# Performance work log

Measured on AMD Instinct MI355X. Metric: run time of the kernel, lower is better.

## Reference

```python
import jax, jax.numpy as jnp
import numpy as np

LN_EPS = 1e-5

def _layernorm(x, gamma, beta):
    mu = jnp.mean(x, axis=-1, keepdims=True)
    var = jnp.var(x, axis=-1, keepdims=True)
    return (x - mu) * jax.lax.rsqrt(var + LN_EPS) * gamma + beta

def setup_inputs() -> dict:
    key = jax.random.key(0)
    ks = jax.random.split(key, 4)
    B, s, d, L = 8, 192, 512, 8
    h = 2048  # embed_dim * 2
    return {
        "lags": jax.random.normal(ks[0], (B, s, d, L), dtype=jnp.float32),
        "gamma1": jnp.ones((d,), jnp.float32),
        "beta1": jnp.zeros((d,), jnp.float32),
        "W1": jax.random.normal(ks[1], (d, h), jnp.float32) * (1.0 / np.sqrt(d)),
        "b1": jnp.zeros((h,), jnp.float32),
        "W2": jax.random.normal(ks[2], (h, d), jnp.float32) * (1.0 / np.sqrt(h)),
        "b2": jnp.zeros((d,), jnp.float32),
        "gamma3": jnp.ones((d,), jnp.float32),
        "beta3": jnp.zeros((d,), jnp.float32),
    }

def reference(lags, gamma1, beta1, W1, b1, W2, b2, gamma3, beta3):
    B, s, d, L = lags.shape
    # (B, s, d, L) -> (B, s, L, d) -> (B, S=s*L, d)
    x = jnp.transpose(lags, (0, 1, 3, 2)).reshape(B, s * L, d)
    scale = 1.0 / jnp.sqrt(jnp.asarray(d, x.dtype))
    # single-head, unprojected attention: scores = X X^T / sqrt(d)
    scores = jnp.einsum('bqd,bkd->bqk', x, x) * scale  # [B, S, S]
    attn = jax.nn.softmax(scores, axis=-1)
    attn_out = jnp.einsum('bqk,bkd->bqd', attn, x)
    q = _layernorm(x + attn_out, gamma1, beta1)
    ff = jnp.dot(jax.nn.gelu(jnp.dot(q, W1) + b1, approximate=False), W2) + b2
    out = _layernorm(q + ff, gamma3, beta3)
    # (B, S, d) -> (B, s, L, d) -> (B, s, d, L)
    return jnp.transpose(out.reshape(B, s, L, d), (0, 1, 3, 2))
```

## Files before the change

### kernel.cpp

```cpp
#include <hip/hip_runtime.h>
#include <hip/hip_bf16.h>
#include <math.h>

#define B_ 8
#define S_ 192
#define D_ 512
#define L_ 8
#define SQ 1536
#define H_ 2048
#define NROW (B_*SQ)
#define SCALE_QK 0.04419417382415922f

typedef unsigned short ushort_t;
typedef unsigned int uint_t;
typedef __attribute__((ext_vector_type(8))) short bf16x8;
typedef __attribute__((ext_vector_type(4))) float f32x4;
typedef __attribute__((ext_vector_type(16))) float f32x16;

__device__ __forceinline__ float bfu2f(ushort_t u) { return __uint_as_float((unsigned)u << 16); }
__device__ __forceinline__ ushort_t f2bfu(float f) {
  __hip_bfloat16 h = __float2bfloat16(f);
  return *reinterpret_cast<ushort_t*>(&h);
}

__device__ __forceinline__ float gelu_tanh(float x) {
  float x2 = x * x;
  float u2 = x * fmaf(0.0713548162f, x2, 1.5957691216f);
  float e = __expf(u2);
  float r = fmaf(-2.0f, __builtin_amdgcn_rcpf(e + 1.0f), 1.0f);
  float hx = 0.5f * x;
  return fmaf(hx, r, hx);
}

__device__ __forceinline__ void gl_lds16(const ushort_t* g, ushort_t* l) {
  __builtin_amdgcn_global_load_lds(
      (const __attribute__((address_space(1))) unsigned int*)g,
      (__attribute__((address_space(3))) unsigned int*)l, 16, 0, 0);
}

#define VMWAIT(N) asm volatile("s_waitcnt vmcnt(" #N ")" ::: "memory")

__global__ __launch_bounds__(256) void k_build_x_f(const float* __restrict__ lags,
                                                   float* __restrict__ x,
                                                   ushort_t* __restrict__ x_bf,
                                                   ushort_t* __restrict__ xT) {
  __shared__ float tile[512][9];
  const int tid = threadIdx.x;
  const float* in = lags + (size_t)blockIdx.x * 4096;
  #pragma unroll
  for (int it = 0; it < 4; ++it) {
    int f = (tid + it * 256) * 4;
    float4 v = *reinterpret_cast<const float4*>(in + f);
    int k = f >> 3, l0 = f & 7;
    tile[k][l0] = v.x; tile[k][l0 + 1] = v.y; tile[k][l0 + 2] = v.z; tile[k][l0 + 3] = v.w;
  }
  __syncthreads();
  const int l = tid >> 5, kbase = tid & 31;
  const size_t r = (size_t)blockIdx.x * 8 + l;
  #pragma unroll
  for (int j = 0; j < 16; ++j) {
    int k = kbase + 32 * j;
    float v = tile[k][l];
    x[r * D_ + k] = v;
    x_bf[r * D_ + k] = f2bfu(v);
  }
  const int b = blockIdx.x / S_, si = blockIdx.x - b * S_;
  #pragma unroll
  for (int dd = 0; dd < 2; ++dd) {
    int d = tid + dd * 256;
    uint_t pk[4];
    #pragma unroll
    for (int j = 0; j < 4; ++j) {
      uint_t lo = f2bfu(tile[d][2 * j]);
      uint_t hi = f2bfu(tile[d][2 * j + 1]);
      pk[j] = (hi << 16) | lo;
    }
    uint_t* dst = (uint_t*)(xT + ((size_t)b * D_ + d) * SQ + si * 8);
    *reinterpret_cast<uint4*>(dst) = make_uint4(pk[0], pk[1], pk[2], pk[3]);
  }
}

__global__ __launch_bounds__(256) void k_wt(const float* __restrict__ W,
                                            ushort_t* __restrict__ Wt,
                                            int K, int N) {
  __shared__ ushort_t tile[64][65];
  int n0 = blockIdx.x * 64, k0 = blockIdx.y * 64;
  for (int i = threadIdx.x; i < 4096; i += 256) {
    int kk = i >> 6, nn = i & 63;
    tile[nn][kk] = f2bfu(W[(size_t)(k0 + kk) * N + n0 + nn]);
  }
  __syncthreads();
  for (int i = threadIdx.x; i < 4096; i += 256) {
    int nn = i >> 6, kk = i & 63;
    Wt[(size_t)(n0 + nn) * K + k0 + kk] = tile[nn][kk];
  }
}

template<int MODE>
__global__ __launch_bounds__(256) void k_gemm(const ushort_t* __restrict__ A,
                                              const ushort_t* __restrict__ Bt,
                                              const float* __restrict__ bias,
                                              void* __restrict__ Cout,
                                              int M, int K, int N,
                                              size_t sAz, size_t sBz, size_t sCz,
                                              float scale) {
  A  += (size_t)blockIdx.z * sAz;
  Bt += (size_t)blockIdx.z * sBz;
  __shared__ ushort_t As0[128 * 64];
  __shared__ ushort_t As1[128 * 64];
  __shared__ ushort_t Bs0[128 * 64];
  __shared__ ushort_t Bs1[128 * 64];
  const int tid = threadIdx.x;
  const int m0 = blockIdx.y * 128, n0 = blockIdx.x * 128;
  const int w = tid >> 6, lane = tid & 63;
  const int wr = w >> 1, wc = w & 1;
  const int l31 = lane & 31, khi = lane >> 5, x7 = lane & 7;
  const int lrow8 = lane >> 3;
  const int cg = ((lane & 7) ^ lrow8) * 8;
  const int lbase = (w * 32) * 64;
  const size_t sK8 = (size_t)8 * K;

  f32x16 acc[2][2];
  if (MODE <= 1) {
    #pragma unroll
    for (int nj = 0; nj < 2; ++nj) {
      float bv = bias[n0 + wc * 64 + nj * 32 + l31];
      #pragma unroll
      for (int mi = 0; mi < 2; ++mi)
        #pragma unroll
        for (int rg = 0; rg < 16; ++rg) acc[mi][nj][rg] = bv;
    }
  } else {
    #pragma unroll
    for (int nj = 0; nj < 2; ++nj)
      #pragma unroll
      for (int mi = 0; mi < 2; ++mi)
        #pragma unroll
        for (int rg = 0; rg < 16; ++rg) acc[mi][nj][rg] = 0.f;
  }

  const ushort_t* gA = A  + (size_t)(m0 + w * 32 + lrow8) * K + cg;
  const ushort_t* gB = Bt + (size_t)(n0 + w * 32 + lrow8) * K + cg;

#define STAGE(AS, BS) do {                                                  \
    ushort_t* la_ = &AS[lbase]; ushort_t* lb_ = &BS[lbase];                 \
    _Pragma("unroll")                                                       \
    for (int j_ = 0; j_ < 4; ++j_) {                                        \
      gl_lds16(gA + (size_t)j_ * sK8, la_ + j_ * 8 * 64);                   \
      gl_lds16(gB + (size_t)j_ * sK8, lb_ + j_ * 8 * 64);                   \
    }                                                                       \
    gA += 64; gB += 64;                                                     \
  } while (0)

#define COMPUTE(AS, BS) do {                                                \
    _Pragma("unroll")                                                       \
    for (int ks_ = 0; ks_ < 4; ++ks_) {                                     \
      const int pos_ = ((ks_ * 2 + khi) ^ x7) * 8;                          \
      bf16x8 af_[2], bf_[2];                                                \
      _Pragma("unroll")                                                     \
      for (int mi_ = 0; mi_ < 2; ++mi_)                                     \
        af_[mi_] = *reinterpret_cast<const bf16x8*>(                        \
            &AS[(wr * 64 + mi_ * 32 + l31) * 64 + pos_]);                   \
      _Pragma("unroll")                                                     \
      for (int nj_ = 0; nj_ < 2; ++nj_)                                     \
        bf_[nj_] = *reinterpret_cast<const bf16x8*>(                        \
            &BS[(wc * 64 + nj_ * 32 + l31) * 64 + pos_]);                   \
      _Pragma("unroll")                                                     \
      for (int mi_ = 0; mi_ < 2; ++mi_)                                     \
        _Pragma("unroll")                                                   \
        for (int nj_ = 0; nj_ < 2; ++nj_)                                   \
          acc[mi_][nj_] = __builtin_amdgcn_mfma_f32_32x32x16_bf16(          \
              af_[mi_], bf_[nj_], acc[mi_][nj_], 0, 0, 0);                  \
    }                                                                       \
  } while (0)

  STAGE(As0, Bs0);
  STAGE(As1, Bs1);

  const int nt = K >> 6;
  for (int t = 0; t < nt - 2; t += 2) {
    VMWAIT(8);
    __builtin_amdgcn_s_barrier();
    COMPUTE(As0, Bs0);
    __builtin_amdgcn_s_barrier();
    STAGE(As0, Bs0);
    VMWAIT(8);
    __builtin_amdgcn_s_barrier();
    COMPUTE(As1, Bs1);
    __builtin_amdgcn_s_barrier();
    STAGE(As1, Bs1);
  }
  VMWAIT(8);
  __builtin_amdgcn_s_barrier();
  COMPUTE(As0, Bs0);
  VMWAIT(0);
  __builtin_amdgcn_s_barrier();
  COMPUTE(As1, Bs1);

#undef STAGE
#undef COMPUTE

  ushort_t* Cb = (ushort_t*)Cout + (size_t)blockIdx.z * sCz;
  float*    Cf = (float*)Cout    + (size_t)blockIdx.z * sCz;
  #pragma unroll
  for (int mi = 0; mi < 2; ++mi)
    #pragma unroll
    for (int nj = 0; nj < 2; ++nj) {
      int gc = n0 + wc * 64 + nj * 32 + l31;
      #pragma unroll
      for (int rg = 0; rg < 16; ++rg) {
        int gr = m0 + wr * 64 + mi * 32 + (rg & 3) + 8 * (rg >> 2) + 4 * khi;
        float v = acc[mi][nj][rg];
        if (MODE == 0) {
          Cb[(size_t)gr * N + gc] = f2bfu(gelu_tanh(v));
        } else if (MODE == 1) {
          Cf[(size_t)gr * N + gc] = v;
        } else if (MODE == 2) {
          Cb[(size_t)gr * N + gc] = f2bfu(v * scale);
        } else {
          Cf[(size_t)gr * N + gc] = v;
        }
      }
    }
}

__global__ __launch_bounds__(256) void k_softmax_bf(ushort_t* __restrict__ sc) {
  uint_t* row = (uint_t*)(sc + (size_t)blockIdx.z * SQ * SQ + (size_t)blockIdx.x * SQ);
  int tid = threadIdx.x;
  __shared__ float red[8];
  float v[6];
  float m = -1e30f;
  #pragma unroll
  for (int k = 0; k < 3; ++k) {
    uint_t u = row[tid + k * 256];
    v[2*k]   = __uint_as_float(u << 16);
    v[2*k+1] = __uint_as_float(u & 0xffff0000u);
    m = fmaxf(m, fmaxf(v[2*k], v[2*k+1]));
  }
  #pragma unroll
  for (int o = 32; o > 0; o >>= 1) m = fmaxf(m, __shfl_down(m, o));
  if ((tid & 63) == 0) red[tid >> 6] = m;
  __syncthreads();
  m = fmaxf(fmaxf(red[0], red[1]), fmaxf(red[2], red[3]));
  __syncthreads();
  float ssum = 0.f;
  #pragma unroll
  for (int k = 0; k < 6; ++k) { v[k] = expf(v[k] - m); ssum += v[k]; }
  #pragma unroll
  for (int o = 32; o > 0; o >>= 1) ssum += __shfl_down(ssum, o);
  if ((tid & 63) == 0) red[4 + (tid >> 6)] = ssum;
  __syncthreads();
  float inv = 1.0f / (red[4] + red[5] + red[6] + red[7]);
  #pragma unroll
  for (int k = 0; k < 3; ++k) {
    uint_t lo = f2bfu(v[2*k] * inv);
    uint_t hi = f2bfu(v[2*k+1] * inv);
    row[tid + k * 256] = (hi << 16) | lo;
  }
}

__global__ __launch_bounds__(256) void k_ln1b(const float* __restrict__ x,
                                              const float* __restrict__ attn,
                                              const float* __restrict__ g,
                                              const float* __restrict__ be,
                                              ushort_t* __restrict__ qbf) {
  size_t base = (size_t)blockIdx.x * D_;
  int tid = threadIdx.x;
  __shared__ float rl[8];
  float v0 = x[base + tid] + attn[base + tid];
  float v1 = x[base + tid + 256] + attn[base + tid + 256];
  float s = v0 + v1, sq = v0 * v0 + v1 * v1;
  #pragma unroll
  for (int o = 32; o > 0; o >>= 1) { s += __shfl_down(s, o); sq += __shfl_down(sq, o); }
  int lane = tid & 63, wid = tid >> 6;
  if (lane == 0) { rl[wid] = s; rl[4 + wid] = sq; }
  __syncthreads();
  s = rl[0] + rl[1] + rl[2] + rl[3];
  sq = rl[4] + rl[5] + rl[6] + rl[7];
  float mean = s * (1.0f / 512.0f);
  float var = sq * (1.0f / 512.0f) - mean * mean;
  float rstd = rsqrtf(var + 1e-5f);
  qbf[base + tid]       = f2bfu((v0 - mean) * rstd * g[tid] + be[tid]);
  qbf[base + tid + 256] = f2bfu((v1 - mean) * rstd * g[tid + 256] + be[tid + 256]);
}

__global__ __launch_bounds__(256) void k_ln3_f(const float* __restrict__ y,
                                               const ushort_t* __restrict__ qbf,
                                               const float* __restrict__ g3,
                                               const float* __restrict__ be3,
                                               float* __restrict__ out) {
  __shared__ float ynorm[8][512];
  const int tid = threadIdx.x;
  const int w = tid >> 6, lane = tid & 63;
  #pragma unroll
  for (int rr = 0; rr < 2; ++rr) {
    int l = 2 * w + rr;
    size_t t = (size_t)blockIdx.x * 8 + l;
    float v[8];
    float s = 0.f, sq = 0.f;
    #pragma unroll
    for (int j = 0; j < 8; ++j) {
      int k = lane + 64 * j;
      v[j] = y[t * D_ + k] + bfu2f(qbf[t * D_ + k]);
      s += v[j]; sq += v[j] * v[j];
    }
    #pragma unroll
    for (int o = 32; o > 0; o >>= 1) { s += __shfl_down(s, o); sq += __shfl_down(sq, o); }
    s = __shfl(s, 0); sq = __shfl(sq, 0);
    float mean = s * (1.0f / 512.0f);
    float var = sq * (1.0f / 512.0f) - mean * mean;
    float rstd = rsqrtf(var + 1e-5f);
    #pragma unroll
    for (int j = 0; j < 8; ++j) {
      int k = lane + 64 * j;
      ynorm[l][k] = (v[j] - mean) * rstd * g3[k] + be3[k];
    }
  }
  __syncthreads();
  float* ob = out + (size_t)blockIdx.x * 4096;
  #pragma unroll
  for (int kk = 0; kk < 2; ++kk) {
    int k = tid * 2 + kk;
    float4 lo = make_float4(ynorm[0][k], ynorm[1][k], ynorm[2][k], ynorm[3][k]);
    float4 hi = make_float4(ynorm[4][k], ynorm[5][k], ynorm[6][k], ynorm[7][k]);
    *reinterpret_cast<float4*>(ob + (size_t)k * 8)     = lo;
    *reinterpret_cast<float4*>(ob + (size_t)k * 8 + 4) = hi;
  }
}

#define TS 64
#define KT 16
__global__ __launch_bounds__(256) void k_build_x_s(const float* __restrict__ lags,
                                                   float* __restrict__ x, int b_base) {
  int idx = blockIdx.x * 256 + threadIdx.x;
  int k = idx & (D_ - 1);
  int r = idx >> 9;
  int b = b_base + r / SQ;
  int t = r - (r / SQ) * SQ;
  int si = t >> 3, l = t & 7;
  size_t src = (((size_t)(b * S_ + si) * D_ + k) << 3) + l;
  x[idx] = lags[src];
}

__global__ __launch_bounds__(256) void k_scores(const float* __restrict__ x,
                                                float* __restrict__ sc, int b_base) {
  const float* A = x;
  float* C = sc;
  __shared__ float As[TS][KT + 1];
  __shared__ float Bs[TS][KT + 1];
  int tx = threadIdx.x & 15, ty = threadIdx.x >> 4;
  int j0 = blockIdx.x * TS, i0 = blockIdx.y * TS;
  float acc[4][4] = {};
  int lk = threadIdx.x & 15, lr = threadIdx.x >> 4;
  for (int k0 = 0; k0 < D_; k0 += KT) {
    #pragma unroll
    for (int it = 0; it < 4; ++it) {
      As[lr + 16 * it][lk] = A[(size_t)(i0 + lr + 16 * it) * D_ + k0 + lk];
      Bs[lr + 16 * it][lk] = A[(size_t)(j0 + lr + 16 * it) * D_ + k0 + lk];
    }
    __syncthreads();
    #pragma unroll
    for (int kk = 0; kk < KT; ++kk) {
      float a[4], bb[4];
      #pragma unroll
      for (int r = 0; r < 4; ++r) a[r] = As[ty * 4 + r][kk];
      #pragma unroll
      for (int c = 0; c < 4; ++c) bb[c] = Bs[tx * 4 + c][kk];
      #pragma unroll
      for (int r = 0; r < 4; ++r)
        #pragma unroll
        for (int c = 0; c < 4; ++c) acc[r][c] = fmaf(a[r], bb[c], acc[r][c]);
    }
    __syncthreads();
  }
  #pragma unroll
  for (int r = 0; r < 4; ++r) {
    float4 v = make_float4(acc[r][0]*SCALE_QK, acc[r][1]*SCALE_QK,
                           acc[r][2]*SCALE_QK, acc[r][3]*SCALE_QK);
    *reinterpret_cast<float4*>(&C[(size_t)(i0 + ty*4 + r) * SQ + j0 + tx*4]) = v;
  }
}

__global__ __launch_bounds__(256) void k_softmax(float* __restrict__ sc) {
  float* row = sc + (size_t)blockIdx.x * SQ;
  int tid = threadIdx.x;
  __shared__ float red[8];
  float m = -1e30f;
  for (int j = tid; j < SQ; j += 256) m = fmaxf(m, row[j]);
  #pragma unroll
  for (int o = 32; o > 0; o >>= 1) m = fmaxf(m, __shfl_down(m, o));
  if ((tid & 63) == 0) red[tid >> 6] = m;
  __syncthreads();
  m = fmaxf(fmaxf(red[0], red[1]), fmaxf(red[2], red[3]));
  __syncthreads();
  float ssum = 0.f;
  for (int j = tid; j < SQ; j += 256) { float e = expf(row[j] - m); row[j] = e; ssum += e; }
  #pragma unroll
  for (int o = 32; o > 0; o >>= 1) ssum += __shfl_down(ssum, o);
  if ((tid & 63) == 0) red[4 + (tid >> 6)] = ssum;
  __syncthreads();
  float inv = 1.0f / (red[4] + red[5] + red[6] + red[7]);
  for (int j = tid; j < SQ; j += 256) row[j] *= inv;
}

__global__ __launch_bounds__(256) void k_attn(const float* __restrict__ x,
                                              const float* __restrict__ sc,
                                              float* __restrict__ attn) {
  const float* X = x;
  const float* P = sc;
  float* O = attn;
  __shared__ float Ps[TS][KT + 1];
  __shared__ float Xs[KT][TS];
  int tx = threadIdx.x & 15, ty = threadIdx.x >> 4;
  int j0 = blockIdx.x * TS, i0 = blockIdx.y * TS;
  float acc[4][4] = {};
  int lk = threadIdx.x & 15, lr = threadIdx.x >> 4;
  int lc = threadIdx.x & 63, lrow = threadIdx.x >> 6;
  for (int k0 = 0; k0 < SQ; k0 += KT) {
    #pragma unroll
    for (int it = 0; it < 4; ++it)
      Ps[lr + 16 * it][lk] = P[(size_t)(i0 + lr + 16 * it) * SQ + k0 + lk];
    #pragma unroll
    for (int it = 0; it < 4; ++it)
      Xs[lrow + 4 * it][lc] = X[(size_t)(k0 + lrow + 4 * it) * D_ + j0 + lc];
    __syncthreads();
    #pragma unroll
    for (int kk = 0; kk < KT; ++kk) {
      float a[4], bb[4];
      #pragma unroll
      for (int r = 0; r < 4; ++r) a[r] = Ps[ty * 4 + r][kk];
      #pragma unroll
      for (int c = 0; c < 4; ++c) bb[c] = Xs[kk][tx * 4 + c];
      #pragma unroll
      for (int r = 0; r < 4; ++r)
        #pragma unroll
        for (int c = 0; c < 4; ++c) acc[r][c] = fmaf(a[r], bb[c], acc[r][c]);
    }
    __syncthreads();
  }
  #pragma unroll
  for (int r = 0; r < 4; ++r) {
    float4 v = make_float4(acc[r][0], acc[r][1], acc[r][2], acc[r][3]);
    *reinterpret_cast<float4*>(&O[(size_t)(i0 + ty*4 + r) * D_ + j0 + tx*4]) = v;
  }
}

__global__ __launch_bounds__(256) void k_ln1(const float* __restrict__ x,
                                             const float* __restrict__ attn,
                                             const float* __restrict__ g,
                                             const float* __restrict__ be,
                                             float* __restrict__ qout) {
  size_t base = (size_t)blockIdx.x * D_;
  int tid = threadIdx.x;
  __shared__ float rl[8];
  float v0 = x[base + tid] + attn[base + tid];
  float v1 = x[base + tid + 256] + attn[base + tid + 256];
  float s = v0 + v1, sq = v0 * v0 + v1 * v1;
  #pragma unroll
  for (int o = 32; o > 0; o >>= 1) { s += __shfl_down(s, o); sq += __shfl_down(sq, o); }
  int lane = tid & 63, wid = tid >> 6;
  if (lane == 0) { rl[wid] = s; rl[4 + wid] = sq; }
  __syncthreads();
  s = rl[0] + rl[1] + rl[2] + rl[3];
  sq = rl[4] + rl[5] + rl[6] + rl[7];
  float mean = s * (1.0f / 512.0f);
  float var = sq * (1.0f / 512.0f) - mean * mean;
  float rstd = rsqrtf(var + 1e-5f);
  qout[base + tid]       = (v0 - mean) * rstd * g[tid] + be[tid];
  qout[base + tid + 256] = (v1 - mean) * rstd * g[tid + 256] + be[tid + 256];
}

__global__ __launch_bounds__(256, 2) void k_ffn(
    const float* __restrict__ q,
    const float* __restrict__ W1, const float* __restrict__ b1,
    const float* __restrict__ W2, const float* __restrict__ b2,
    const float* __restrict__ g3, const float* __restrict__ be3,
    float* __restrict__ out, int row_base)
{
  __shared__ float qs[8][D_];
  __shared__ float mid[8][H_];
  const int tid = threadIdx.x;
  const int row0 = blockIdx.x * 8;
  for (int idx = tid; idx < 8 * D_; idx += 256)
    qs[idx >> 9][idx & (D_ - 1)] = q[(size_t)row0 * D_ + idx];
  __syncthreads();
  float acc[8][8];
  {
    float4 bA = *reinterpret_cast<const float4*>(b1 + (tid << 3));
    float4 bB = *reinterpret_cast<const float4*>(b1 + (tid << 3) + 4);
    float bv[8] = {bA.x, bA.y, bA.z, bA.w, bB.x, bB.y, bB.z, bB.w};
    #pragma unroll
    for (int jj = 0; jj < 8; ++jj)
      #pragma unroll
      for (int r = 0; r < 8; ++r) acc[jj][r] = bv[jj];
  }
  for (int k4 = 0; k4 < D_ / 4; ++k4) {
    float4 qv[8];
    #pragma unroll
    for (int r = 0; r < 8; ++r)
      qv[r] = *reinterpret_cast<const float4*>(&qs[r][k4 << 2]);
    #pragma unroll
    for (int kk = 0; kk < 4; ++kk) {
      const int k = (k4 << 2) + kk;
      float4 wA = *reinterpret_cast<const float4*>(W1 + (size_t)k * H_ + (tid << 3));
      float4 wB = *reinterpret_cast<const float4*>(W1 + (size_t)k * H_ + (tid << 3) + 4);
      float wv[8] = {wA.x, wA.y, wA.z, wA.w, wB.x, wB.y, wB.z, wB.w};
      #pragma unroll
      for (int r = 0; r < 8; ++r) {
        float qk = (kk == 0) ? qv[r].x : (kk == 1) ? qv[r].y : (kk == 2) ? qv[r].z : qv[r].w;
        #pragma unroll
        for (int jj = 0; jj < 8; ++jj) acc[jj][r] = fmaf(qk, wv[jj], acc[jj][r]);
      }
    }
  }
  #pragma unroll
  for (int jj = 0; jj < 8; ++jj)
    #pragma unroll
    for (int r = 0; r < 8; ++r) {
      float v = acc[jj][r];
      mid[r][(tid << 3) + jj] = 0.5f * v * (1.0f + erff(v * 0.70710678118654752f));
    }
  __syncthreads();
  float acc2[8][2];
  {
    float b20 = b2[tid << 1], b21 = b2[(tid << 1) + 1];
    #pragma unroll
    for (int r = 0; r < 8; ++r) { acc2[r][0] = b20; acc2[r][1] = b21; }
  }
  for (int j4 = 0; j4 < H_ / 4; ++j4) {
    float4 mv[8];
    #pragma unroll
    for (int r = 0; r < 8; ++r)
      mv[r] = *reinterpret_cast<const float4*>(&mid[r][j4 << 2]);
    #pragma unroll
    for (int kk = 0; kk < 4; ++kk) {
      const int j = (j4 << 2) + kk;
      float2 wv = *reinterpret_cast<const float2*>(W2 + (size_t)j * D_ + (tid << 1));
      #pragma unroll
      for (int r = 0; r < 8; ++r) {
        float m = (kk == 0) ? mv[r].x : (kk == 1) ? mv[r].y : (kk == 2) ? mv[r].z : mv[r].w;
        acc2[r][0] = fmaf(m, wv.x, acc2[r][0]);
        acc2[r][1] = fmaf(m, wv.y, acc2[r][1]);
      }
    }
  }
  __syncthreads();
  float* ys = &mid[0][0];
  #pragma unroll
  for (int r = 0; r < 8; ++r) {
    ys[r * D_ + (tid << 1)]     = qs[r][(tid << 1)]     + acc2[r][0];
    ys[r * D_ + (tid << 1) + 1] = qs[r][(tid << 1) + 1] + acc2[r][1];
  }
  __syncthreads();
  float g3a = g3[tid],  g3b = g3[tid + 256];
  float be3a = be3[tid], be3b = be3[tid + 256];
  float* rl = &qs[0][0];
  for (int r = 0; r < 8; ++r) {
    float v0 = ys[r * D_ + tid], v1 = ys[r * D_ + tid + 256];
    float s = v0 + v1, sq = v0 * v0 + v1 * v1;
    #pragma unroll
    for (int o = 32; o > 0; o >>= 1) { s += __shfl_down(s, o); sq += __shfl_down(sq, o); }
    int lane = tid & 63, wid = tid >> 6;
    if (lane == 0) { rl[wid] = s; rl[4 + wid] = sq; }
    __syncthreads();
    s = rl[0] + rl[1] + rl[2] + rl[3];
    sq = rl[4] + rl[5] + rl[6] + rl[7];
    __syncthreads();
    float mean = s * (1.0f / 512.0f);
    float var = sq * (1.0f / 512.0f) - mean * mean;
    float rstd = rsqrtf(var + 1e-5f);
    int t = row_base + row0 + r;
    int b = t / SQ, tt = t - b * SQ;
    int si = tt >> 3, l = tt & 7;
    size_t ob = (((size_t)(b * S_ + si) * D_) << 3) + l;
    out[ob + ((size_t)tid << 3)]         = (v0 - mean) * rstd * g3a + be3a;
    out[ob + ((size_t)(tid + 256) << 3)] = (v1 - mean) * rstd * g3b + be3b;
  }
}

extern "C" void kernel_launch(void* const* d_in, const int* in_sizes, int n_in,
                              void* d_out, int out_size, void* d_ws, size_t ws_size,
                              hipStream_t stream) {
  const float* lags   = (const float*)d_in[0];
  const float* gamma1 = (const float*)d_in[1];
  const float* beta1  = (const float*)d_in[2];
  const float* W1     = (const float*)d_in[3];
  const float* b1     = (const float*)d_in[4];
  const float* W2     = (const float*)d_in[5];
  const float* b2     = (const float*)d_in[6];
  const float* g3     = (const float*)d_in[7];
  const float* be3    = (const float*)d_in[8];
  float* out = (float*)d_out;

  float* ws = (float*)d_ws;
  const size_t NX  = (size_t)B_ * SQ * D_;
  const size_t NXB = (size_t)SQ * D_;
  const size_t NS  = (size_t)SQ * SQ;

  const size_t need_full = (3 * NX + 8 * NS) * sizeof(float);

  if (ws_size >= need_full) {
    float* x        = ws;
    float* attn     = x + NX;
    ushort_t* q_bf  = (ushort_t*)(attn + NX);
    ushort_t* w1t   = q_bf + NX;
    ushort_t* w2t   = w1t + (size_t)H_ * D_;
    ushort_t* region = w2t + (size_t)H_ * D_;
    ushort_t* sc_bf = region;
    ushort_t* x_bf  = region + 8 * NS;
    ushort_t* xT_bf = x_bf + NX;
    ushort_t* mid_bf = region;

    k_build_x_f<<<dim3(B_ * S_), 256, 0, stream>>>(lags, x, x_bf, xT_bf);
    k_wt<<<dim3(H_ / 64, D_ / 64), 256, 0, stream>>>(W1, w1t, D_, H_);
    k_wt<<<dim3(D_ / 64, H_ / 64), 256, 0, stream>>>(W2, w2t, H_, D_);
    k_gemm<2><<<dim3(SQ / 128, SQ / 128, B_), 256, 0, stream>>>(
        x_bf, x_bf, nullptr, sc_bf, SQ, D_, SQ, NXB, NXB, NS, SCALE_QK);
    k_softmax_bf<<<dim3(SQ, 1, B_), 256, 0, stream>>>(sc_bf);
    k_gemm<3><<<dim3(D_ / 128, SQ / 128, B_), 256, 0, stream>>>(
        sc_bf, xT_bf, nullptr, attn, SQ, SQ, D_, NS, NXB, NXB, 1.0f);
    k_ln1b<<<dim3(NROW), 256, 0, stream>>>(x, attn, gamma1, beta1, q_bf);
    k_gemm<0><<<dim3(H_ / 128, NROW / 128, 1), 256, 0, stream>>>(
        q_bf, w1t, b1, mid_bf, NROW, D_, H_, 0, 0, 0, 1.0f);
    k_gemm<1><<<dim3(D_ / 128, NROW / 128, 1), 256, 0, stream>>>(
        mid_bf, w2t, b2, attn, NROW, H_, D_, 0, 0, 0, 1.0f);
    k_ln3_f<<<dim3(B_ * S_), 256, 0, stream>>>(attn, q_bf, g3, be3, out);
  } else {
    float* xb   = ws;
    float* sc   = xb + NXB;
    float* atb  = sc + NS;
    float* qb   = atb + NXB;
    for (int b = 0; b < B_; ++b) {
      k_build_x_s<<<dim3((unsigned)(NXB / 256)), 256, 0, stream>>>(lags, xb, b);
      k_scores<<<dim3(SQ / TS, SQ / TS, 1), 256, 0, stream>>>(xb, sc, b);
      k_softmax<<<dim3(SQ, 1, 1), 256, 0, stream>>>(sc);
      k_attn<<<dim3(D_ / TS, SQ / TS, 1), 256, 0, stream>>>(xb, sc, atb);
      k_ln1<<<dim3(SQ), 256, 0, stream>>>(xb, atb, gamma1, beta1, qb);
      k_ffn<<<dim3(SQ / 8), 256, 0, stream>>>(qb, W1, b1, W2, b2, g3, be3, out, b * SQ);
    }
  }
}
```

Measured before the change: 298.0 us.

## Use 256x128 tiles, 3-stage pipeline, 16x16 MFMA and XCD-aware block remap in GEMMs

Replaces the 128x128 two-buffer GEMM with a 512-thread kernel computing 256x128 tiles. It uses a triple-buffered LDS pipeline with a single barrier per k-step, 16x16x32 bf16 MFMA instead of 32x32x16, and a block-index swizzle that groups tiles by XCD. The aim is to raise operand reuse per block and overlap global loads with compute better. The cost is more LDS per block (144 KB), which lowers occupancy, and fewer blocks for the small attention GEMMs, which may underfill the CUs.

```diff
diff --git a/kernel.cpp b/kernel.cpp
--- a/kernel.cpp
+++ b/kernel.cpp
@@ -15,7 +15,6 @@
 typedef unsigned int uint_t;
 typedef __attribute__((ext_vector_type(8))) short bf16x8;
 typedef __attribute__((ext_vector_type(4))) float f32x4;
-typedef __attribute__((ext_vector_type(16))) float f32x16;
 
 __device__ __forceinline__ float bfu2f(ushort_t u) { return __uint_as_float((unsigned)u << 16); }
 __device__ __forceinline__ ushort_t f2bfu(float f) {
@@ -97,120 +96,122 @@
 }
 
 template<int MODE>
-__global__ __launch_bounds__(256) void k_gemm(const ushort_t* __restrict__ A,
-                                              const ushort_t* __restrict__ Bt,
-                                              const float* __restrict__ bias,
-                                              void* __restrict__ Cout,
-                                              int M, int K, int N,
-                                              size_t sAz, size_t sBz, size_t sCz,
-                                              float scale) {
+__global__ __launch_bounds__(512) void k_gemm2(const ushort_t* __restrict__ A,
+                                               const ushort_t* __restrict__ Bt,
+                                               const float* __restrict__ bias,
+                                               void* __restrict__ Cout,
+                                               int M, int K, int N,
+                                               size_t sAz, size_t sBz, size_t sCz,
+                                               float scale) {
   A  += (size_t)blockIdx.z * sAz;
   Bt += (size_t)blockIdx.z * sBz;
-  __shared__ ushort_t As0[128 * 64];
-  __shared__ ushort_t As1[128 * 64];
+  __shared__ ushort_t As0[256 * 64];
+  __shared__ ushort_t As1[256 * 64];
+  __shared__ ushort_t As2[256 * 64];
   __shared__ ushort_t Bs0[128 * 64];
   __shared__ ushort_t Bs1[128 * 64];
+  __shared__ ushort_t Bs2[128 * 64];
+
+  const int gx = gridDim.x;
+  const int nwg = gx * gridDim.y;
+  int lin = blockIdx.y * gx + blockIdx.x;
+  lin = (lin & 7) * (nwg >> 3) + (lin >> 3);
+  const int n0 = (lin % gx) * 128;
+  const int m0 = (lin / gx) * 256;
+
   const int tid = threadIdx.x;
-  const int m0 = blockIdx.y * 128, n0 = blockIdx.x * 128;
   const int w = tid >> 6, lane = tid & 63;
-  const int wr = w >> 1, wc = w & 1;
-  const int l31 = lane & 31, khi = lane >> 5, x7 = lane & 7;
+  const int wm = w >> 1, wn = w & 1;
+  const int l15 = lane & 15, quad = lane >> 4;
   const int lrow8 = lane >> 3;
   const int cg = ((lane & 7) ^ lrow8) * 8;
-  const int lbase = (w * 32) * 64;
-  const size_t sK8 = (size_t)8 * K;
-
-  f32x16 acc[2][2];
+  const int xsw = l15 & 7;
+  const size_t sK64 = (size_t)64 * K;
+
+  f32x4 acc[4][4];
   if (MODE <= 1) {
     #pragma unroll
-    for (int nj = 0; nj < 2; ++nj) {
-      float bv = bias[n0 + wc * 64 + nj * 32 + l31];
-      #pragma unroll
-      for (int mi = 0; mi < 2; ++mi)
-        #pragma unroll
-        for (int rg = 0; rg < 16; ++rg) acc[mi][nj][rg] = bv;
+    for (int nj = 0; nj < 4; ++nj) {
+      float bv = bias[n0 + wn * 64 + nj * 16 + l15];
+      #pragma unroll
+      for (int mi = 0; mi < 4; ++mi) acc[mi][nj] = (f32x4){bv, bv, bv, bv};
     }
   } else {
     #pragma unroll
-    for (int nj = 0; nj < 2; ++nj)
-      #pragma unroll
-      for (int mi = 0; mi < 2; ++mi)
-        #pragma unroll
-        for (int rg = 0; rg < 16; ++rg) acc[mi][nj][rg] = 0.f;
-  }
-
-  const ushort_t* gA = A  + (size_t)(m0 + w * 32 + lrow8) * K + cg;
-  const ushort_t* gB = Bt + (size_t)(n0 + w * 32 + lrow8) * K + cg;
-
-#define STAGE(AS, BS) do {                                                  \
-    ushort_t* la_ = &AS[lbase]; ushort_t* lb_ = &BS[lbase];                 \
-    _Pragma("unroll")                                                       \
-    for (int j_ = 0; j_ < 4; ++j_) {                                        \
-      gl_lds16(gA + (size_t)j_ * sK8, la_ + j_ * 8 * 64);                   \
-      gl_lds16(gB + (size_t)j_ * sK8, lb_ + j_ * 8 * 64);                   \
-    }                                                                       \
-    gA += 64; gB += 64;                                                     \
+    for (int nj = 0; nj < 4; ++nj)
+      #pragma unroll
+      for (int mi = 0; mi < 4; ++mi) acc[mi][nj] = (f32x4){0.f, 0.f, 0.f, 0.f};
+  }
+
+  const ushort_t* pA = A  + (size_t)(m0 + w * 8 + lrow8) * K + cg;
+  const ushort_t* pB = Bt + (size_t)(n0 + w * 8 + lrow8) * K + cg;
+  const int lb = (w * 8) * 64;
+
+#define STAGE(TT, AS, BS) do {                                              \
+    const size_t ko_ = (size_t)(TT) * 64;                                   \
+    gl_lds16(pA + ko_,             &AS[lb]);                                \
+    gl_lds16(pA + ko_ +     sK64,  &AS[lb + 64 * 64]);                      \
+    gl_lds16(pA + ko_ + 2 * sK64,  &AS[lb + 128 * 64]);                     \
+    gl_lds16(pA + ko_ + 3 * sK64,  &AS[lb + 192 * 64]);                     \
+    gl_lds16(pB + ko_,             &BS[lb]);                                \
+    gl_lds16(pB + ko_ +     sK64,  &BS[lb + 64 * 64]);                      \
   } while (0)
 
 #define COMPUTE(AS, BS) do {                                                \
     _Pragma("unroll")                                                       \
-    for (int ks_ = 0; ks_ < 4; ++ks_) {                                     \
-      const int pos_ = ((ks_ * 2 + khi) ^ x7) * 8;                          \
-      bf16x8 af_[2], bf_[2];                                                \
+    for (int kk_ = 0; kk_ < 2; ++kk_) {                                     \
+      const int csel_ = ((kk_ * 4 + quad) ^ xsw) * 8;                       \
+      bf16x8 af_[4], bf_[4];                                                \
       _Pragma("unroll")                                                     \
-      for (int mi_ = 0; mi_ < 2; ++mi_)                                     \
+      for (int mi_ = 0; mi_ < 4; ++mi_)                                     \
         af_[mi_] = *reinterpret_cast<const bf16x8*>(                        \
-            &AS[(wr * 64 + mi_ * 32 + l31) * 64 + pos_]);                   \
+            &AS[(wm * 64 + mi_ * 16 + l15) * 64 + csel_]);                  \
       _Pragma("unroll")                                                     \
-      for (int nj_ = 0; nj_ < 2; ++nj_)                                     \
+      for (int nj_ = 0; nj_ < 4; ++nj_)                                     \
         bf_[nj_] = *reinterpret_cast<const bf16x8*>(                        \
-            &BS[(wc * 64 + nj_ * 32 + l31) * 64 + pos_]);                   \
+            &BS[(wn * 64 + nj_ * 16 + l15) * 64 + csel_]);                  \
       _Pragma("unroll")                                                     \
-      for (int mi_ = 0; mi_ < 2; ++mi_)                                     \
+      for (int mi_ = 0; mi_ < 4; ++mi_)                                     \
         _Pragma("unroll")                                                   \
-        for (int nj_ = 0; nj_ < 2; ++nj_)                                   \
-          acc[mi_][nj_] = __builtin_amdgcn_mfma_f32_32x32x16_bf16(          \
+        for (int nj_ = 0; nj_ < 4; ++nj_)                                   \
+          acc[mi_][nj_] = __builtin_amdgcn_mfma_f32_16x16x32_bf16(          \
               af_[mi_], bf_[nj_], acc[mi_][nj_], 0, 0, 0);                  \
     }                                                                       \
   } while (0)
 
-  STAGE(As0, Bs0);
-  STAGE(As1, Bs1);
+#define STEP(TT, CA, CB, NA, NB) do {                                       \
+    if ((TT) < nt) {                                                        \
+      if ((TT) == nt - 1) { VMWAIT(0); } else { VMWAIT(6); }                \
+      __builtin_amdgcn_s_barrier();                                         \
+      if ((TT) + 2 < nt) STAGE((TT) + 2, NA, NB);                           \
+      COMPUTE(CA, CB);                                                      \
+    }                                                                       \
+  } while (0)
 
   const int nt = K >> 6;
-  for (int t = 0; t < nt - 2; t += 2) {
-    VMWAIT(8);
-    __builtin_amdgcn_s_barrier();
-    COMPUTE(As0, Bs0);
-    __builtin_amdgcn_s_barrier();
-    STAGE(As0, Bs0);
-    VMWAIT(8);
-    __builtin_amdgcn_s_barrier();
-    COMPUTE(As1, Bs1);
-    __builtin_amdgcn_s_barrier();
-    STAGE(As1, Bs1);
-  }
-  VMWAIT(8);
-  __builtin_amdgcn_s_barrier();
-  COMPUTE(As0, Bs0);
-  VMWAIT(0);
-  __builtin_amdgcn_s_barrier();
-  COMPUTE(As1, Bs1);
+  STAGE(0, As0, Bs0);
+  STAGE(1, As1, Bs1);
+  for (int t = 0; t < nt; t += 3) {
+    STEP(t,     As0, Bs0, As2, Bs2);
+    STEP(t + 1, As1, Bs1, As0, Bs0);
+    STEP(t + 2, As2, Bs2, As1, Bs1);
+  }
 
 #undef STAGE
 #undef COMPUTE
+#undef STEP
 
   ushort_t* Cb = (ushort_t*)Cout + (size_t)blockIdx.z * sCz;
   float*    Cf = (float*)Cout    + (size_t)blockIdx.z * sCz;
   #pragma unroll
-  for (int mi = 0; mi < 2; ++mi)
-    #pragma unroll
-    for (int nj = 0; nj < 2; ++nj) {
-      int gc = n0 + wc * 64 + nj * 32 + l31;
-      #pragma unroll
-      for (int rg = 0; rg < 16; ++rg) {
-        int gr = m0 + wr * 64 + mi * 32 + (rg & 3) + 8 * (rg >> 2) + 4 * khi;
-        float v = acc[mi][nj][rg];
+  for (int mi = 0; mi < 4; ++mi)
+    #pragma unroll
+    for (int nj = 0; nj < 4; ++nj) {
+      int gc = n0 + wn * 64 + nj * 16 + l15;
+      #pragma unroll
+      for (int r = 0; r < 4; ++r) {
+        int gr = m0 + wm * 64 + mi * 16 + quad * 4 + r;
+        float v = acc[mi][nj][r];
         if (MODE == 0) {
           Cb[(size_t)gr * N + gc] = f2bfu(gelu_tanh(v));
         } else if (MODE == 1) {
@@ -614,15 +615,15 @@
     k_build_x_f<<<dim3(B_ * S_), 256, 0, stream>>>(lags, x, x_bf, xT_bf);
     k_wt<<<dim3(H_ / 64, D_ / 64), 256, 0, stream>>>(W1, w1t, D_, H_);
     k_wt<<<dim3(D_ / 64, H_ / 64), 256, 0, stream>>>(W2, w2t, H_, D_);
-    k_gemm<2><<<dim3(SQ / 128, SQ / 128, B_), 256, 0, stream>>>(
+    k_gemm2<2><<<dim3(SQ / 128, SQ / 256, B_), 512, 0, stream>>>(
         x_bf, x_bf, nullptr, sc_bf, SQ, D_, SQ, NXB, NXB, NS, SCALE_QK);
     k_softmax_bf<<<dim3(SQ, 1, B_), 256, 0, stream>>>(sc_bf);
-    k_gemm<3><<<dim3(D_ / 128, SQ / 128, B_), 256, 0, stream>>>(
+    k_gemm2<3><<<dim3(D_ / 128, SQ / 256, B_), 512, 0, stream>>>(
         sc_bf, xT_bf, nullptr, attn, SQ, SQ, D_, NS, NXB, NXB, 1.0f);
     k_ln1b<<<dim3(NROW), 256, 0, stream>>>(x, attn, gamma1, beta1, q_bf);
-    k_gemm<0><<<dim3(H_ / 128, NROW / 128, 1), 256, 0, stream>>>(
+    k_gemm2<0><<<dim3(H_ / 128, NROW / 256, 1), 512, 0, stream>>>(
         q_bf, w1t, b1, mid_bf, NROW, D_, H_, 0, 0, 0, 1.0f);
-    k_gemm<1><<<dim3(D_ / 128, NROW / 128, 1), 256, 0, stream>>>(
+    k_gemm2<1><<<dim3(D_ / 128, NROW / 256, 1), 512, 0, stream>>>(
         mid_bf, w2t, b2, attn, NROW, H_, D_, 0, 0, 0, 1.0f);
     k_ln3_f<<<dim3(B_ * S_), 256, 0, stream>>>(attn, q_bf, g3, be3, out);
   } else {
```

Measured after the change: 302.3 us. Within noise of the previous version (+1.4%).
